# Kernel tuning notes

Measured on AMD Instinct MI355X. Metric: run time of the kernel, lower is better.

The kernel has to match this reference:

```python
import jax, jax.numpy as jnp
import numpy as np

CHUNK = 32
PRIOR = 64
POSE = 512
PRED = 128
B = 2048


def setup_inputs() -> dict:
    key = jax.random.key(0)
    k1, k2, k3, k4, k5, k6 = jax.random.split(key, 6)
    initial_feature = jax.random.normal(k1, (B, PRIOR, POSE), dtype=jnp.float32)
    pred_feature = jax.random.normal(k2, (B, PRED, POSE), dtype=jnp.float32)
    s1 = 1.0 / np.sqrt(CHUNK * POSE)
    s2 = 1.0 / np.sqrt(POSE)
    W1 = jax.random.uniform(k3, (POSE, CHUNK * POSE), minval=-s1, maxval=s1, dtype=jnp.float32)
    b1 = jax.random.uniform(k4, (POSE,), minval=-s1, maxval=s1, dtype=jnp.float32)
    W2 = jax.random.uniform(k5, (POSE, POSE), minval=-s2, maxval=s2, dtype=jnp.float32)
    b2 = jax.random.uniform(k6, (POSE,), minval=-s2, maxval=s2, dtype=jnp.float32)
    return {"initial_feature": initial_feature, "pred_feature": pred_feature,
            "W1": W1, "b1": b1, "W2": W2, "b2": b2}


def reference(initial_feature, pred_feature, W1, b1, W2, b2):
    Bn = initial_feature.shape[0]
    # last CHUNK prior frames flattened -> [B, CHUNK*POSE]
    x = initial_feature[:, PRIOR - CHUNK:, :].reshape(Bn, -1)
    # spatial_chunk_encoder (Dropout is identity in eval mode)
    mem = (x @ W1.T + b1) @ W2.T + b2          # [B, POSE]
    head = pred_feature[:, :CHUNK, :]          # [B, CHUNK, POSE]
    score = jnp.einsum('bd,bcd->bc', mem, head)  # per-token dot product
    g = jax.nn.sigmoid(score)[..., None]       # [B, CHUNK, 1]
    blended = g * head + (1.0 - g) * mem[:, None, :]
    return pred_feature.at[:, :CHUNK, :].set(blended)
```

## Files before the change

kernel.cpp:

```cpp
#include <hip/hip_runtime.h>
#include <hip/hip_bf16.h>
#include <stdint.h>

#define CHUNKC 32
#define PRIORC 64
#define POSEC 512
#define PREDC 128
#define NB 2048
#define K1 (CHUNKC*POSEC)
#define KS 8
#define KCH (K1/KS)

typedef __attribute__((ext_vector_type(8))) short bf16x8;
typedef __attribute__((ext_vector_type(8))) unsigned short u16x8;
typedef __attribute__((ext_vector_type(4))) float f32x4;
typedef __attribute__((ext_vector_type(4))) float f4v;

__device__ __forceinline__ unsigned short f2b(float f) {
    union { float f; unsigned int u; } x; x.f = f;
    unsigned int r = x.u + 0x7fffu + ((x.u >> 16) & 1u);
    return (unsigned short)(r >> 16);
}
__device__ __forceinline__ float b2f(unsigned short u) {
    union { unsigned int i; float f; } x; x.i = ((unsigned int)u) << 16; return x.f;
}
__device__ __forceinline__ unsigned short cf(float f) {
    __hip_bfloat16 h = __float2bfloat16(f);
    union { __hip_bfloat16 h; unsigned short u; } x; x.h = h; return x.u;
}

__device__ __forceinline__ void gload_lds16(const void* g, void* l) {
    __builtin_amdgcn_global_load_lds(
        (const __attribute__((address_space(1))) unsigned int*)g,
        (__attribute__((address_space(3))) unsigned int*)l, 16, 0, 0);
}

#define W1N4  2097152
#define W2N4  65536
__global__ __launch_bounds__(256) void cvt_w_kernel(const float4* __restrict__ W1,
                                                    const float4* __restrict__ W2,
                                                    ushort4* __restrict__ w1b,
                                                    ushort4* __restrict__ w2b) {
    const int64_t n = W1N4 + W2N4;
    const int64_t stride = (int64_t)gridDim.x * blockDim.x;
    for (int64_t i = (int64_t)blockIdx.x * blockDim.x + threadIdx.x; i < n; i += stride) {
        float4 v; ushort4* dst;
        if (i < W1N4) { v = W1[i]; dst = w1b + i; }
        else          { v = W2[i - W1N4]; dst = w2b + (i - W1N4); }
        *dst = make_ushort4(f2b(v.x), f2b(v.y), f2b(v.z), f2b(v.w));
    }
}

__global__ __launch_bounds__(512) void gemm1_kernel(const float* __restrict__ init,
                                                    const ushort* __restrict__ w1b,
                                                    ushort* __restrict__ part) {
    __shared__ float  As[2][128][64];
    __shared__ ushort Bs[2][256][64];
    const int t = threadIdx.x;
    const int l = t & 63, wid = t >> 6;
    const int wr = wid >> 2, wc = wid & 3;
    const int orig = (blockIdx.x & 7) * 32 + (blockIdx.x >> 3);
    const int mt = orig & 15, nt = (orig >> 4) & 1, ks = orig >> 5;
    const int NIT = KCH / 64;

    f32x4 acc[4][4] = {};

    const float*  aG = init + (int64_t)(mt * 128) * 32768 + 16384 + ks * KCH;
    const ushort* bG = w1b + (int64_t)(nt * 256) * K1 + ks * KCH;

    const int arow  = t >> 4;
    const int aslot = (t & 15) ^ ((t >> 4) & 15);
    const int brow = t >> 3;
    const int bcol = ((t & 7) ^ ((t >> 3) & 7)) * 8;

    const int fr = l & 15, fq = l >> 4;
    const int cxB = fr & 7;

    auto STAGE = [&](int buf, int k0) {
#pragma unroll
        for (int i = 0; i < 4; ++i)
            gload_lds16(aG + (int64_t)(i * 32 + arow) * 32768 + k0 + aslot * 4,
                        (char*)&As[buf][0][0] + i * 8192 + wid * 1024);
#pragma unroll
        for (int i = 0; i < 4; ++i)
            gload_lds16(bG + (int64_t)(i * 64 + brow) * K1 + k0 + bcol,
                        (char*)&Bs[buf][0][0] + i * 8192 + wid * 1024);
    };

    STAGE(0, 0);

    for (int it = 0; it < NIT; ++it) {
        const int cur = it & 1;
        if (it + 1 < NIT) {
            STAGE(cur ^ 1, (it + 1) * 64);
            asm volatile("s_waitcnt vmcnt(8)" ::: "memory");
        } else {
            asm volatile("s_waitcnt vmcnt(0)" ::: "memory");
        }
        __builtin_amdgcn_s_barrier();
        asm volatile("" ::: "memory");
        __builtin_amdgcn_sched_barrier(0);
#pragma unroll
        for (int k2 = 0; k2 < 2; ++k2) {
            bf16x8 a[4], b[4];
            const int s0 = k2 * 8 + fq * 2;
#pragma unroll
            for (int m = 0; m < 4; ++m) {
                const int r = wr * 64 + m * 16 + fr;
                f32x4 va = *(const f32x4*)&As[cur][r][((s0    ) ^ fr) * 4];
                f32x4 vb = *(const f32x4*)&As[cur][r][((s0 + 1) ^ fr) * 4];
                u16x8 w;
                w[0] = cf(va[0]); w[1] = cf(va[1]); w[2] = cf(va[2]); w[3] = cf(va[3]);
                w[4] = cf(vb[0]); w[5] = cf(vb[1]); w[6] = cf(vb[2]); w[7] = cf(vb[3]);
                union { u16x8 u; bf16x8 b; } cvtu; cvtu.u = w;
                a[m] = cvtu.b;
            }
            const int cs = ((k2 * 4 + fq) ^ cxB) * 8;
#pragma unroll
            for (int n = 0; n < 4; ++n)
                b[n] = *(const bf16x8*)&Bs[cur][wc * 64 + n * 16 + fr][cs];
#pragma unroll
            for (int m = 0; m < 4; ++m)
#pragma unroll
                for (int n = 0; n < 4; ++n)
                    acc[m][n] = __builtin_amdgcn_mfma_f32_16x16x32_bf16(a[m], b[n], acc[m][n], 0, 0, 0);
        }
        asm volatile("" ::: "memory");
        __builtin_amdgcn_s_barrier();
    }

    ushort* P = part + (int64_t)ks * NB * POSEC;
    const int mbase = mt * 128 + wr * 64, nbase = nt * 256 + wc * 64;
#pragma unroll
    for (int m = 0; m < 4; ++m)
#pragma unroll
        for (int n = 0; n < 4; ++n) {
            int row0 = mbase + m * 16 + fq * 4;
            int col  = nbase + n * 16 + fr;
#pragma unroll
            for (int r = 0; r < 4; ++r)
                P[(int64_t)(row0 + r) * POSEC + col] = f2b(acc[m][n][r]);
        }
}

__global__ __launch_bounds__(256) void reduce_kernel(const ushort* __restrict__ part,
                                                     const float* __restrict__ b1,
                                                     u16x8* __restrict__ A2) {
    const int gid = blockIdx.x * 256 + threadIdx.x;
    const int64_t e0 = (int64_t)gid * 8;
    float s[8] = {};
#pragma unroll
    for (int k = 0; k < KS; ++k) {
        u16x8 p = *(const u16x8*)(part + (int64_t)k * (NB * POSEC) + e0);
#pragma unroll
        for (int j = 0; j < 8; ++j) s[j] += b2f(p[j]);
    }
    const int col = (int)(e0 & 511);
    f4v b0 = *(const f4v*)&b1[col];
    f4v b4 = *(const f4v*)&b1[col + 4];
    u16x8 o;
#pragma unroll
    for (int j = 0; j < 4; ++j) { o[j] = f2b(s[j] + b0[j]); o[j+4] = f2b(s[j+4] + b4[j]); }
    A2[gid] = o;
}

__global__ __launch_bounds__(256) void gemm2_kernel(const ushort* __restrict__ A2,
                                                    const ushort* __restrict__ w2b,
                                                    const float* __restrict__ b2,
                                                    float* __restrict__ mem) {
    __shared__ ushort As[64][64];
    __shared__ ushort Bs[64][64];
    const int t = threadIdx.x;
    const int l = t & 63, wid = t >> 6;
    const int wr = wid >> 1, wc = wid & 1;
    const int mt = blockIdx.x >> 3, nt = blockIdx.x & 7;

    f32x4 acc[2][2] = {};
    const ushort* aG = A2  + (int64_t)(mt * 64) * POSEC;
    const ushort* bG = w2b + (int64_t)(nt * 64) * POSEC;
    const int srow = t >> 3;
    const int scol = (((t & 7) ^ ((t >> 3) & 7))) * 8;
    const int fr = l & 15, fq = l >> 4;
    const int cx = fr & 7;

    for (int k0 = 0; k0 < POSEC; k0 += 64) {
#pragma unroll
        for (int i = 0; i < 2; ++i) {
            gload_lds16(aG + (int64_t)(i * 32 + srow) * POSEC + k0 + scol,
                        (char*)&As[0][0] + i * 4096 + wid * 1024);
            gload_lds16(bG + (int64_t)(i * 32 + srow) * POSEC + k0 + scol,
                        (char*)&Bs[0][0] + i * 4096 + wid * 1024);
        }
        __syncthreads();
#pragma unroll
        for (int k2 = 0; k2 < 2; ++k2) {
            const int cs = ((k2 * 4 + fq) ^ cx) * 8;
            bf16x8 a[2], b[2];
#pragma unroll
            for (int m = 0; m < 2; ++m)
                a[m] = *(const bf16x8*)&As[wr * 32 + m * 16 + fr][cs];
#pragma unroll
            for (int n = 0; n < 2; ++n)
                b[n] = *(const bf16x8*)&Bs[wc * 32 + n * 16 + fr][cs];
#pragma unroll
            for (int m = 0; m < 2; ++m)
#pragma unroll
                for (int n = 0; n < 2; ++n)
                    acc[m][n] = __builtin_amdgcn_mfma_f32_16x16x32_bf16(a[m], b[n], acc[m][n], 0, 0, 0);
        }
        __syncthreads();
    }

    const int mbase = mt * 64 + wr * 32, nbase = nt * 64 + wc * 32;
#pragma unroll
    for (int m = 0; m < 2; ++m)
#pragma unroll
        for (int n = 0; n < 2; ++n) {
            int row0 = mbase + m * 16 + fq * 4;
            int col  = nbase + n * 16 + fr;
            float bias = b2[col];
#pragma unroll
            for (int r = 0; r < 4; ++r)
                mem[(int64_t)(row0 + r) * POSEC + col] = acc[m][n][r] + bias;
        }
}

__global__ __launch_bounds__(256) void blend_kernel(const float* __restrict__ pred,
                                                    const float* __restrict__ mem,
                                                    float* __restrict__ out) {
    const int b = blockIdx.x;
    const int t = threadIdx.x;
    __shared__ float sm[POSEC];
    __shared__ float sg[CHUNKC];

    sm[t]       = mem[(int64_t)b * POSEC + t];
    sm[t + 256] = mem[(int64_t)b * POSEC + 256 + t];
    __syncthreads();

    const int l = t & 63, wid = t >> 6;
    const float4* sm4 = (const float4*)sm;
    const float4* p4 = (const float4*)pred + (int64_t)b * 16384;
    float4* o4 = (float4*)out + (int64_t)b * 16384;

#pragma unroll
    for (int ci = 0; ci < 8; ++ci) {
        int c = wid * 8 + ci;
        float4 h0 = p4[c * 128 + l * 2];
        float4 h1 = p4[c * 128 + l * 2 + 1];
        float4 m0 = sm4[l * 2];
        float4 m1 = sm4[l * 2 + 1];
        float s = h0.x * m0.x + h0.y * m0.y + h0.z * m0.z + h0.w * m0.w
                + h1.x * m1.x + h1.y * m1.y + h1.z * m1.z + h1.w * m1.w;
#pragma unroll
        for (int o = 32; o; o >>= 1) s += __shfl_xor(s, o);
        if (l == 0) sg[c] = 1.0f / (1.0f + expf(-s));
    }
    __syncthreads();

#pragma unroll
    for (int i = 0; i < 16; ++i) {
        int idx = i * 256 + t;
        int row = idx >> 7, c4 = idx & 127;
        float g = sg[row];
        float4 h = p4[idx];
        float4 m = sm4[c4];
        float4 r;
        r.x = g * h.x + (1.0f - g) * m.x;
        r.y = g * h.y + (1.0f - g) * m.y;
        r.z = g * h.z + (1.0f - g) * m.z;
        r.w = g * h.w + (1.0f - g) * m.w;
        o4[idx] = r;
    }
#pragma unroll
    for (int i = 0; i < 48; ++i) {
        int idx = 4096 + i * 256 + t;
        f4v h = __builtin_nontemporal_load((const f4v*)p4 + idx);
        __builtin_nontemporal_store(h, (f4v*)o4 + idx);
    }
}


extern "C" void kernel_launch(void* const* d_in, const int* in_sizes, int n_in,
                              void* d_out, int out_size, void* d_ws, size_t ws_size,
                              hipStream_t stream) {
    const float* init = (const float*)d_in[0];
    const float* pred = (const float*)d_in[1];
    const float* W1   = (const float*)d_in[2];
    const float* b1   = (const float*)d_in[3];
    const float* W2   = (const float*)d_in[4];
    const float* b2   = (const float*)d_in[5];
    float* out = (float*)d_out;

    char* ws = (char*)d_ws;
    ushort* w1b  = (ushort*)(ws);
    ushort* w2b  = (ushort*)(ws + 16777216);
    ushort* part = (ushort*)(ws + 17301504);
    ushort* A2   = (ushort*)(ws + 34078720);
    float*  mem  = (float*) (ws + 36175872);

    cvt_w_kernel<<<1024, 256, 0, stream>>>((const float4*)W1, (const float4*)W2,
                                           (ushort4*)w1b, (ushort4*)w2b);
    gemm1_kernel<<<256, 512, 0, stream>>>(init, w1b, part);
    reduce_kernel<<<512, 256, 0, stream>>>(part, b1, (u16x8*)A2);
    gemm2_kernel<<<256, 256, 0, stream>>>(A2, w2b, b2, mem);
    blend_kernel<<<NB, 256, 0, stream>>>(pred, mem, out);
}
```

Baseline: 288.5 us.

## Deepen gemm1 LDS pipeline to four stages with half-width K tiles

Switches the gemm1 main loop from a double-buffered 64-wide K tile to a four-stage ring of 32-wide K tiles, keeping three loads in flight ahead of compute. Swizzle patterns and the vmcnt waits are adjusted to the new tile shape. The aim is to hide more global memory latency at the same LDS footprint. The cost is twice as many barriers per unit of K and less MFMA work per iteration between them.

```diff
diff --git a/kernel.cpp b/kernel.cpp
--- a/kernel.cpp
+++ b/kernel.cpp
@@ -54,71 +54,75 @@
 __global__ __launch_bounds__(512) void gemm1_kernel(const float* __restrict__ init,
                                                     const ushort* __restrict__ w1b,
                                                     ushort* __restrict__ part) {
-    __shared__ float  As[2][128][64];
-    __shared__ ushort Bs[2][256][64];
+    __shared__ float  As[4][128][32];
+    __shared__ ushort Bs[4][256][32];
     const int t = threadIdx.x;
     const int l = t & 63, wid = t >> 6;
     const int wr = wid >> 2, wc = wid & 3;
     const int orig = (blockIdx.x & 7) * 32 + (blockIdx.x >> 3);
     const int mt = orig & 15, nt = (orig >> 4) & 1, ks = orig >> 5;
-    const int NIT = KCH / 64;
+    const int NIT = KCH / 32;
 
     f32x4 acc[4][4] = {};
 
     const float*  aG = init + (int64_t)(mt * 128) * 32768 + 16384 + ks * KCH;
     const ushort* bG = w1b + (int64_t)(nt * 256) * K1 + ks * KCH;
 
-    const int arow  = t >> 4;
-    const int aslot = (t & 15) ^ ((t >> 4) & 15);
-    const int brow = t >> 3;
-    const int bcol = ((t & 7) ^ ((t >> 3) & 7)) * 8;
+    const int arow  = t >> 3;
+    const int aslot = (t & 7) ^ ((t >> 3) & 7);
+    const int brow = t >> 2;
+    const int bslot = (t & 3) ^ ((t >> 2) & 3);
 
     const int fr = l & 15, fq = l >> 4;
-    const int cxB = fr & 7;
+    const int axk = fr & 7;
+    const int bxk = fr & 3;
 
     auto STAGE = [&](int buf, int k0) {
 #pragma unroll
-        for (int i = 0; i < 4; ++i)
-            gload_lds16(aG + (int64_t)(i * 32 + arow) * 32768 + k0 + aslot * 4,
+        for (int i = 0; i < 2; ++i)
+            gload_lds16(aG + (int64_t)(i * 64 + arow) * 32768 + k0 + aslot * 4,
                         (char*)&As[buf][0][0] + i * 8192 + wid * 1024);
 #pragma unroll
-        for (int i = 0; i < 4; ++i)
-            gload_lds16(bG + (int64_t)(i * 64 + brow) * K1 + k0 + bcol,
+        for (int i = 0; i < 2; ++i)
+            gload_lds16(bG + (int64_t)(i * 128 + brow) * K1 + k0 + bslot * 8,
                         (char*)&Bs[buf][0][0] + i * 8192 + wid * 1024);
     };
 
-    STAGE(0, 0);
+    STAGE(0, 0); STAGE(1, 32); STAGE(2, 64);
 
     for (int it = 0; it < NIT; ++it) {
-        const int cur = it & 1;
-        if (it + 1 < NIT) {
-            STAGE(cur ^ 1, (it + 1) * 64);
+        const int cur = it & 3;
+        if (it + 3 < NIT) {
+            STAGE((it + 3) & 3, (it + 3) * 32);
+            asm volatile("s_waitcnt vmcnt(12)" ::: "memory");
+        } else if (it + 2 < NIT) {
             asm volatile("s_waitcnt vmcnt(8)" ::: "memory");
+        } else if (it + 1 < NIT) {
+            asm volatile("s_waitcnt vmcnt(4)" ::: "memory");
         } else {
             asm volatile("s_waitcnt vmcnt(0)" ::: "memory");
         }
         __builtin_amdgcn_s_barrier();
         asm volatile("" ::: "memory");
         __builtin_amdgcn_sched_barrier(0);
-#pragma unroll
-        for (int k2 = 0; k2 < 2; ++k2) {
+        {
             bf16x8 a[4], b[4];
-            const int s0 = k2 * 8 + fq * 2;
 #pragma unroll
             for (int m = 0; m < 4; ++m) {
                 const int r = wr * 64 + m * 16 + fr;
-                f32x4 va = *(const f32x4*)&As[cur][r][((s0    ) ^ fr) * 4];
-                f32x4 vb = *(const f32x4*)&As[cur][r][((s0 + 1) ^ fr) * 4];
+                f32x4 va = *(const f32x4*)&As[cur][r][((fq * 2    ) ^ axk) * 4];
+                f32x4 vb = *(const f32x4*)&As[cur][r][((fq * 2 + 1) ^ axk) * 4];
                 u16x8 w;
                 w[0] = cf(va[0]); w[1] = cf(va[1]); w[2] = cf(va[2]); w[3] = cf(va[3]);
                 w[4] = cf(vb[0]); w[5] = cf(vb[1]); w[6] = cf(vb[2]); w[7] = cf(vb[3]);
                 union { u16x8 u; bf16x8 b; } cvtu; cvtu.u = w;
                 a[m] = cvtu.b;
             }
-            const int cs = ((k2 * 4 + fq) ^ cxB) * 8;
-#pragma unroll
-            for (int n = 0; n < 4; ++n)
-                b[n] = *(const bf16x8*)&Bs[cur][wc * 64 + n * 16 + fr][cs];
+#pragma unroll
+            for (int n = 0; n < 4; ++n) {
+                const int r = wc * 64 + n * 16 + fr;
+                b[n] = *(const bf16x8*)&Bs[cur][r][(fq ^ bxk) * 8];
+            }
 #pragma unroll
             for (int m = 0; m < 4; ++m)
 #pragma unroll
```

New measurement: 315.6 us. 1.09x slower.
